# Performance work log

Hardware: AMD Instinct MI355X
Metric: run time of the kernel (lower is better)

The kernel has to match this reference:

```python
import jax, jax.numpy as jnp
import numpy as np

K = 16
NUM_CLASSES = 1000
TAU = 0.2
LOGIT_SCALE = 20.0


def setup_inputs() -> dict:
    key = jax.random.key(0)
    k1, k2, k3, k4, k5 = jax.random.split(key, 5)
    B, D, N = 2048, 256, 100000
    x = jax.random.normal(k1, (B, D), dtype=jnp.float32)
    mean = jax.random.normal(k2, (D,), dtype=jnp.float32)
    std = jax.random.uniform(k3, (D,), dtype=jnp.float32, minval=0.5, maxval=1.5)
    mem_features = jax.random.normal(k4, (N, D), dtype=jnp.float32)
    mem_labels = jax.random.randint(k5, (N,), 0, NUM_CLASSES)
    return {"x": x, "mean": mean, "std": std,
            "mem_features": mem_features, "mem_labels": mem_labels}


def reference(x, mean, std, mem_features, mem_labels):
    # preprocess: standardize then L2-normalize rows (eval mode, no noise)
    x = (x - mean) / std
    norm = jnp.maximum(jnp.linalg.norm(x, axis=1, keepdims=True), 1e-6)
    x = x / norm
    # dense cosine similarity: [B, N]
    sims = jnp.einsum('bd,nd->bn', x, mem_features)
    # top-k neighbors per query
    top_sims, top_idx = jax.lax.top_k(sims, K)          # [B, K]
    top_lbl = mem_labels[top_idx]                       # [B, K]
    weights = jax.nn.softmax(top_sims / max(1e-6, TAU), axis=1)
    # scatter-add softmax weights into class logits
    B = x.shape[0]
    rows = jnp.arange(B)[:, None]                       # [B, 1]
    logits = jnp.zeros((B, NUM_CLASSES), dtype=x.dtype).at[rows, top_lbl].add(weights)
    return logits * LOGIT_SCALE
```

## Files before the change

### kernel.cpp

```cpp
#include <hip/hip_runtime.h>
#include <math.h>

constexpr int BQ   = 2048;
constexpr int D    = 256;
constexpr int NMEM = 100000;
constexpr int TOPK = 16;
constexpr int NCLS = 1000;
constexpr float TAU = 0.2f;
constexpr float LOGIT_SCALE = 20.0f;

constexpr int KTOT = 256;
constexpr int BK   = 64;
constexpr int TM   = 128;
constexpr int TN   = 128;
constexpr int CTILES = 13;
constexpr int CHUNK  = TN * CTILES;
constexpr int NCH    = 64;
constexpr int RBLK   = BQ / TM;
constexpr int NBLK   = RBLK * NCH;
constexpr int TOTAL_IT = CTILES * (KTOT / BK);
constexpr float XSCALE = 16.0f;
constexpr float INV_XS = 0.0625f;
constexpr float THR    = 3.0f;
constexpr float THRS   = 48.0f;
constexpr int CAP    = 512;
constexpr int MSEL   = 64;
constexpr int SELCAP = 96;
constexpr float NEG  = -3.0e38f;

using i32x4  = __attribute__((ext_vector_type(4))) int;
using i32x8  = __attribute__((ext_vector_type(8))) int;
using f32x16 = __attribute__((ext_vector_type(16))) float;

__device__ __forceinline__ unsigned f2e4m3(float f) {
    const unsigned u = __float_as_uint(f);
    const unsigned s = (u >> 24) & 0x80u;
    const int e = (int)((u >> 23) & 0xff);
    int te = e - 120;
    if (te <= 0) return s;
    const unsigned m = u & 0x7fffffu;
    const unsigned r = m + 0x7ffffu + ((m >> 20) & 1u);
    unsigned keep;
    if (r & 0x800000u) { ++te; keep = 0; } else keep = (r >> 20) & 7u;
    if (te >= 16 || (te == 15 && keep == 7)) return s | 0x7eu;
    return s | ((unsigned)te << 3) | keep;
}

__device__ __forceinline__ void load_lds16(const void* g, void* l) {
    __builtin_amdgcn_global_load_lds((const __attribute__((address_space(1))) void*)g,
                                     (__attribute__((address_space(3))) void*)l,
                                     16, 0, 0);
}

__global__ __launch_bounds__(256) void knn_prep(
    const float* __restrict__ x, const float* __restrict__ mean,
    const float* __restrict__ stdv, unsigned char* __restrict__ A1,
    float* __restrict__ XN, int* __restrict__ cnt)
{
    const int row = blockIdx.x;
    const int t = threadIdx.x;
    float v = (x[row * D + t] - mean[t]) / stdv[t];
    float s = v * v;
    #pragma unroll
    for (int off = 32; off > 0; off >>= 1) s += __shfl_down(s, off, 64);
    __shared__ float wsum[4];
    __shared__ float nrm;
    const int lane = t & 63, wid = t >> 6;
    if (lane == 0) wsum[wid] = s;
    __syncthreads();
    if (t == 0) {
        nrm = fmaxf(sqrtf(wsum[0] + wsum[1] + wsum[2] + wsum[3]), 1e-6f);
        cnt[row] = 0;
    }
    __syncthreads();
    const float xnv = v / nrm;
    A1[(size_t)row * KTOT + t] = (unsigned char)f2e4m3(xnv * XSCALE);
    XN[(size_t)row * D + t] = xnv;
}

__global__ __launch_bounds__(256) void knn_convb(
    const float* __restrict__ mem, unsigned char* __restrict__ B1)
{
    const int tid = threadIdx.x;
    const int rloc = tid >> 5, t = tid & 31;
    const long n = (long)blockIdx.x * 8 + rloc;
    if (n >= NMEM) return;
    const float* src = mem + n * D + t * 8;
    const float4 v0 = *(const float4*)(src);
    const float4 v1 = *(const float4*)(src + 4);
    const float f[8] = {v0.x, v0.y, v0.z, v0.w, v1.x, v1.y, v1.z, v1.w};
    unsigned long long pk = 0;
    #pragma unroll
    for (int i = 0; i < 8; ++i)
        pk |= (unsigned long long)f2e4m3(f[i]) << (8 * i);
    *(unsigned long long*)(B1 + n * KTOT + t * 8) = pk;
}

__global__ __launch_bounds__(256, 4) void knn_gemm_topk(
    const unsigned char* __restrict__ A1, const unsigned char* __restrict__ B1,
    int* __restrict__ cnt, uint2* __restrict__ cand_buf)
{
    __shared__ alignas(16) unsigned char As[2][TM * BK];
    __shared__ alignas(16) unsigned char Bs[2][TN * BK];

    const int tid  = threadIdx.x;
    const int lane = tid & 63, wave = tid >> 6;
    const int wm = wave >> 1, wn = wave & 1;
    const int l31 = lane & 31;
    const int kb  = lane >> 5;

    const int nblk = blockIdx.x;
    const int xcd = nblk & 7, bi = nblk >> 3;
    const int rb = bi & 15;
    const int ch = (bi >> 4) + 8 * xcd;
    const int row0  = rb * TM;
    const int cbase = ch * CHUNK;

    int aoff[2][2], boff[2][2];
    #pragma unroll
    for (int ti = 0; ti < 2; ++ti) {
        const int ar = wm * 64 + ti * 32 + l31;
        const int br = wn * 64 + ti * 32 + l31;
        #pragma unroll
        for (int c = 0; c < 2; ++c) {
            aoff[ti][c] = ar * BK + (((2 * kb + c) - (ar >> 1)) & 3) * 16;
            boff[ti][c] = br * BK + (((2 * kb + c) - (br >> 1)) & 3) * 16;
        }
    }

    const unsigned char* aSrc[2];
    int cSub[2], bSeg[2];
    #pragma unroll
    for (int s = 0; s < 2; ++s) {
        const int ci = s * 256 + tid;
        const int r = ci >> 2, sl = ci & 3;
        aSrc[s] = A1 + (size_t)(row0 + r) * KTOT + (((sl + (r >> 1)) & 3) << 4);
        cSub[s] = r;
        bSeg[s] = ((sl + (r >> 1)) & 3) << 4;
    }
    const unsigned char* bB[2];
    auto computeBB = [&](int tile) {
        #pragma unroll
        for (int s = 0; s < 2; ++s) {
            int candi = cbase + tile * TN + cSub[s];
            if (candi >= NMEM) candi = NMEM - 1;
            bB[s] = B1 + (size_t)candi * KTOT + bSeg[s];
        }
    };

    f32x16 acc[2][2];
    #pragma unroll
    for (int i = 0; i < 2; ++i)
        #pragma unroll
        for (int j = 0; j < 2; ++j)
            #pragma unroll
            for (int r = 0; r < 16; ++r) acc[i][j][r] = 0.f;

    int t = 0, kk = 0, p = 0;
    computeBB(0);
    {
        #pragma unroll
        for (int s = 0; s < 2; ++s)
            load_lds16(aSrc[s], (char*)As[0] + s * 4096 + wave * 1024);
        #pragma unroll
        for (int s = 0; s < 2; ++s)
            load_lds16(bB[s], (char*)Bs[0] + s * 4096 + wave * 1024);
    }
    __syncthreads();

    for (int it = 0; it < TOTAL_IT; ++it) {
        const bool last = (kk == KTOT - BK);
        const int tn = last ? t + 1 : t;
        const int kn = last ? 0 : kk + BK;

        const unsigned char* Ab = As[p];
        const unsigned char* Bb = Bs[p];
        i32x8 Afr[2], Bfr[2];
        #pragma unroll
        for (int ti = 0; ti < 2; ++ti) {
            const i32x4 alo = *(const i32x4*)(Ab + aoff[ti][0]);
            const i32x4 ahi = *(const i32x4*)(Ab + aoff[ti][1]);
            Afr[ti] = __builtin_shufflevector(alo, ahi, 0, 1, 2, 3, 4, 5, 6, 7);
            const i32x4 blo = *(const i32x4*)(Bb + boff[ti][0]);
            const i32x4 bhi = *(const i32x4*)(Bb + boff[ti][1]);
            Bfr[ti] = __builtin_shufflevector(blo, bhi, 0, 1, 2, 3, 4, 5, 6, 7);
        }

        if (tn < CTILES) {
            if (last) computeBB(tn);
            #pragma unroll
            for (int s = 0; s < 2; ++s)
                load_lds16(aSrc[s] + kn, (char*)As[p ^ 1] + s * 4096 + wave * 1024);
            #pragma unroll
            for (int s = 0; s < 2; ++s)
                load_lds16(bB[s] + kn, (char*)Bs[p ^ 1] + s * 4096 + wave * 1024);
        }

        #pragma unroll
        for (int ti = 0; ti < 2; ++ti)
            #pragma unroll
            for (int tj = 0; tj < 2; ++tj)
                acc[ti][tj] = __builtin_amdgcn_mfma_scale_f32_32x32x64_f8f6f4(
                    Afr[ti], Bfr[tj], acc[ti][tj], 0, 0,
                    0, 0x7f7f7f7f, 0, 0x7f7f7f7f);

        __syncthreads();

        if (last) {
            const int tb = cbase + t * TN;
            #pragma unroll
            for (int ti = 0; ti < 2; ++ti) {
                const int rb0 = row0 + wm * 64 + ti * 32 + 4 * kb;
                #pragma unroll
                for (int tj = 0; tj < 2; ++tj) {
                    const int cidx = tb + wn * 64 + tj * 32 + l31;
                    #pragma unroll
                    for (int r = 0; r < 16; ++r) {
                        const float v = acc[ti][tj][r];
                        if (v > THRS && cidx < NMEM) {
                            const int rg = rb0 + (r & 3) + 8 * (r >> 2);
                            const int pos = atomicAdd(&cnt[rg], 1);
                            if (pos < CAP)
                                cand_buf[(size_t)rg * CAP + pos] =
                                    make_uint2(__float_as_uint(v * INV_XS),
                                               (unsigned)cidx);
                        }
                        acc[ti][tj][r] = 0.f;
                    }
                }
            }
        }
        t = tn; kk = kn; p ^= 1;
    }
}

__global__ __launch_bounds__(256) void knn_final(
    const int* __restrict__ cnt, const uint2* __restrict__ cand_buf,
    const float* __restrict__ xn, const float* __restrict__ mem,
    const int* __restrict__ labels, float* __restrict__ out)
{
    constexpr float BSCALE = 200.0f;
    __shared__ float cls[NCLS];
    __shared__ uint2 cl[CAP];
    __shared__ int   hist[1024];
    __shared__ int   psum[256];
    __shared__ float tstar;
    __shared__ int   scount;
    __shared__ int   seli[SELCAP];
    __shared__ float ex[SELCAP];
    __shared__ float fs[TOPK];
    __shared__ int   fi[TOPK];
    __shared__ float zshare;

    const int row = blockIdx.x;
    const int tid = threadIdx.x;
    const int lane = tid & 63, w = tid >> 6;

    const float4 xr = *(const float4*)(xn + (size_t)row * D + lane * 4);

    for (int c = tid; c < NCLS; c += 256) cls[c] = 0.f;
    for (int i = tid; i < 1024; i += 256) hist[i] = 0;
    int n = cnt[row]; if (n > CAP) n = CAP;
    for (int i = tid; i < n; i += 256) cl[i] = cand_buf[(size_t)row * CAP + i];
    if (tid == 0) scount = 0;
    __syncthreads();

    for (int i = tid; i < n; i += 256) {
        const float v = __uint_as_float(cl[i].x);
        int b = (int)((v - THR) * BSCALE);
        b = max(0, min(1023, b));
        atomicAdd(&hist[b], 1);
    }
    __syncthreads();
    psum[tid] = hist[4 * tid] + hist[4 * tid + 1] + hist[4 * tid + 2] + hist[4 * tid + 3];
    __syncthreads();
    if (tid == 0) {
        int cum = 0, g = 255;
        for (; g >= 0; --g) {
            if (cum + psum[g] >= MSEL) break;
            cum += psum[g];
        }
        float t = THR;
        if (g >= 0) {
            int bb = 4 * g + 3;
            for (; bb > 4 * g; --bb) {
                cum += hist[bb];
                if (cum >= MSEL) break;
            }
            if (bb == 4 * g) cum += hist[bb];
            t = THR + (float)bb * (1.0f / BSCALE);
        }
        tstar = t;
    }
    __syncthreads();
    for (int i = tid; i < n; i += 256) {
        const float v = __uint_as_float(cl[i].x);
        if (v >= tstar) {
            const int p = atomicAdd(&scount, 1);
            if (p < SELCAP) seli[p] = (int)cl[i].y;
        }
    }
    __syncthreads();
    int ns = scount; if (ns > SELCAP) ns = SELCAP;

    for (int c = w; c < ns; c += 4) {
        const float4 mv = *(const float4*)(mem + (size_t)seli[c] * D + lane * 4);
        float s = xr.x * mv.x + xr.y * mv.y + xr.z * mv.z + xr.w * mv.w;
        #pragma unroll
        for (int off = 32; off > 0; off >>= 1) s += __shfl_down(s, off, 64);
        if (lane == 0) ex[c] = s;
    }
    __syncthreads();

    if (tid == 0) {
        float kmin = NEG; int kslot = 0;
        #pragma unroll
        for (int s = 0; s < TOPK; ++s) { fs[s] = NEG; fi[s] = -1; }
        for (int c = 0; c < ns; ++c) {
            const float v = ex[c];
            if (v > kmin) {
                fs[kslot] = v; fi[kslot] = seli[c];
                kmin = fs[0]; kslot = 0;
                #pragma unroll
                for (int s = 1; s < TOPK; ++s) {
                    const float tq = fs[s];
                    if (tq < kmin) { kmin = tq; kslot = s; }
                }
            }
        }
        float smax = fs[0];
        #pragma unroll
        for (int s = 1; s < TOPK; ++s) smax = fmaxf(smax, fs[s]);
        float e[TOPK]; float Z = 0.f;
        #pragma unroll
        for (int s = 0; s < TOPK; ++s) {
            e[s] = (fi[s] >= 0) ? expf((fs[s] - smax) * (1.0f / TAU)) : 0.f;
            Z += e[s];
        }
        for (int s = 0; s < TOPK; ++s) {
            if (fi[s] >= 0) cls[labels[fi[s]]] += e[s];
        }
        zshare = Z;
    }
    __syncthreads();
    const float scale = LOGIT_SCALE / zshare;
    for (int c = tid; c < NCLS; c += 256)
        out[(size_t)row * NCLS + c] = cls[c] * scale;
}

extern "C" void kernel_launch(void* const* d_in, const int* in_sizes, int n_in,
                              void* d_out, int out_size, void* d_ws, size_t ws_size,
                              hipStream_t stream) {
    (void)in_sizes; (void)n_in; (void)out_size; (void)ws_size;
    const float* x    = (const float*)d_in[0];
    const float* mean = (const float*)d_in[1];
    const float* stdv = (const float*)d_in[2];
    const float* mem  = (const float*)d_in[3];
    const int*   lbl  = (const int*)d_in[4];
    float* out = (float*)d_out;

    unsigned char* A1 = (unsigned char*)d_ws;
    float* XN = (float*)(A1 + (size_t)BQ * KTOT);
    unsigned char* B1 = (unsigned char*)(XN + (size_t)BQ * D);
    int* cnt = (int*)(B1 + (size_t)NMEM * KTOT);
    uint2* cand = (uint2*)(cnt + BQ);

    knn_prep<<<BQ, 256, 0, stream>>>(x, mean, stdv, A1, XN, cnt);
    knn_convb<<<(NMEM + 7) / 8, 256, 0, stream>>>(mem, B1);
    knn_gemm_topk<<<NBLK, 256, 0, stream>>>(A1, B1, cnt, cand);
    knn_final<<<BQ, 256, 0, stream>>>(cnt, cand, XN, mem, lbl, out);
}
```

Before: 381.4 us.

## Triple-buffer LDS staging with prefetch distance two and rebalance chunk grid

Replaces the double-buffered LDS pipeline with a three-stage ring that prefetches two K-steps ahead. It uses explicit vmcnt waits plus raw s_barrier in place of __syncthreads, so one outstanding load group can stay in flight across the barrier. Chunks per row block drop from 64 to 48 while tiles per chunk grow from 13 to 17, giving fewer, longer blocks, and occupancy is lowered to 3 blocks per CU to fit the extra LDS. The hand-written waitcnt only guards ordering if the compiler issues the async LDS loads in the expected order.

```diff
diff --git a/kernel.cpp b/kernel.cpp
--- a/kernel.cpp
+++ b/kernel.cpp
@@ -13,9 +13,9 @@
 constexpr int BK   = 64;
 constexpr int TM   = 128;
 constexpr int TN   = 128;
-constexpr int CTILES = 13;
+constexpr int CTILES = 17;
 constexpr int CHUNK  = TN * CTILES;
-constexpr int NCH    = 64;
+constexpr int NCH    = 48;
 constexpr int RBLK   = BQ / TM;
 constexpr int NBLK   = RBLK * NCH;
 constexpr int TOTAL_IT = CTILES * (KTOT / BK);
@@ -96,12 +96,12 @@
     *(unsigned long long*)(B1 + n * KTOT + t * 8) = pk;
 }
 
-__global__ __launch_bounds__(256, 4) void knn_gemm_topk(
+__global__ __launch_bounds__(256, 3) void knn_gemm_topk(
     const unsigned char* __restrict__ A1, const unsigned char* __restrict__ B1,
     int* __restrict__ cnt, uint2* __restrict__ cand_buf)
 {
-    __shared__ alignas(16) unsigned char As[2][TM * BK];
-    __shared__ alignas(16) unsigned char Bs[2][TN * BK];
+    __shared__ alignas(16) unsigned char As[3][TM * BK];
+    __shared__ alignas(16) unsigned char Bs[3][TN * BK];
 
     const int tid  = threadIdx.x;
     const int lane = tid & 63, wave = tid >> 6;
@@ -112,7 +112,7 @@
     const int nblk = blockIdx.x;
     const int xcd = nblk & 7, bi = nblk >> 3;
     const int rb = bi & 15;
-    const int ch = (bi >> 4) + 8 * xcd;
+    const int ch = (bi >> 4) + 6 * xcd;
     const int row0  = rb * TM;
     const int cbase = ch * CHUNK;
 
@@ -147,6 +147,14 @@
             bB[s] = B1 + (size_t)candi * KTOT + bSeg[s];
         }
     };
+    auto stage = [&](int buf, int kofs) {
+        #pragma unroll
+        for (int s = 0; s < 2; ++s)
+            load_lds16(aSrc[s] + kofs, (char*)As[buf] + s * 4096 + wave * 1024);
+        #pragma unroll
+        for (int s = 0; s < 2; ++s)
+            load_lds16(bB[s] + kofs, (char*)Bs[buf] + s * 4096 + wave * 1024);
+    };
 
     f32x16 acc[2][2];
     #pragma unroll
@@ -156,23 +164,15 @@
             #pragma unroll
             for (int r = 0; r < 16; ++r) acc[i][j][r] = 0.f;
 
-    int t = 0, kk = 0, p = 0;
     computeBB(0);
-    {
-        #pragma unroll
-        for (int s = 0; s < 2; ++s)
-            load_lds16(aSrc[s], (char*)As[0] + s * 4096 + wave * 1024);
-        #pragma unroll
-        for (int s = 0; s < 2; ++s)
-            load_lds16(bB[s], (char*)Bs[0] + s * 4096 + wave * 1024);
-    }
-    __syncthreads();
-
+    stage(0, 0);
+    stage(1, 64);
+    asm volatile("s_waitcnt vmcnt(4)" ::: "memory");
+    __builtin_amdgcn_sched_barrier(0);
+    __builtin_amdgcn_s_barrier();
+
+    int p = 0;
     for (int it = 0; it < TOTAL_IT; ++it) {
-        const bool last = (kk == KTOT - BK);
-        const int tn = last ? t + 1 : t;
-        const int kn = last ? 0 : kk + BK;
-
         const unsigned char* Ab = As[p];
         const unsigned char* Bb = Bs[p];
         i32x8 Afr[2], Bfr[2];
@@ -186,14 +186,12 @@
             Bfr[ti] = __builtin_shufflevector(blo, bhi, 0, 1, 2, 3, 4, 5, 6, 7);
         }
 
-        if (tn < CTILES) {
-            if (last) computeBB(tn);
-            #pragma unroll
-            for (int s = 0; s < 2; ++s)
-                load_lds16(aSrc[s] + kn, (char*)As[p ^ 1] + s * 4096 + wave * 1024);
-            #pragma unroll
-            for (int s = 0; s < 2; ++s)
-                load_lds16(bB[s] + kn, (char*)Bs[p ^ 1] + s * 4096 + wave * 1024);
+        const int is = it + 2;
+        const bool have2 = (is < TOTAL_IT);
+        if (have2) {
+            if ((is & 3) == 0) computeBB(is >> 2);
+            int pn = p + 2; if (pn >= 3) pn -= 3;
+            stage(pn, (is & 3) << 6);
         }
 
         #pragma unroll
@@ -204,9 +202,8 @@
                     Afr[ti], Bfr[tj], acc[ti][tj], 0, 0,
                     0, 0x7f7f7f7f, 0, 0x7f7f7f7f);
 
-        __syncthreads();
-
-        if (last) {
+        if ((it & 3) == 3) {
+            const int t = it >> 2;
             const int tb = cbase + t * TN;
             #pragma unroll
             for (int ti = 0; ti < 2; ++ti) {
@@ -230,7 +227,17 @@
                 }
             }
         }
-        t = tn; kk = kn; p ^= 1;
+
+        if (it < TOTAL_IT - 1) {
+            if (have2) {
+                asm volatile("s_waitcnt vmcnt(4)" ::: "memory");
+            } else {
+                asm volatile("s_waitcnt vmcnt(0)" ::: "memory");
+            }
+            __builtin_amdgcn_sched_barrier(0);
+            __builtin_amdgcn_s_barrier();
+        }
+        ++p; if (p >= 3) p = 0;
     }
 }
 
```

New measurement: 369.8 us. -3.0%, faster.
